# Kernel tuning notes

Hardware: AMD Instinct MI355X
Metric: run time of the kernel (lower is better)

## Reference

```python
import jax, jax.numpy as jnp
import numpy as np

N, A, M = 2, 360, 512
NP, PS = 32, 64


def _rampfilter(size):
    n = np.concatenate((np.arange(1, size / 2 + 1, 2, dtype=int),
                        np.arange(size / 2 - 1, 0, -2, dtype=int)))
    f = np.zeros(size)
    f[0] = 0.25
    f[1::2] = -1 / (np.pi * n) ** 2
    return 2 * np.real(np.fft.fft(f))


def setup_inputs() -> dict:
    rng = np.random.default_rng(0)
    sino = rng.standard_normal((N, 1, A, M))
    # ramp filtering (done in __init__ of the torch module, filtered=True)
    final_width = max(64, int(2 ** np.ceil(np.log2(2 * M))))
    pad = final_width - M
    filt = _rampfilter(final_width)
    sino_p = np.pad(sino, ((0, 0), (0, 0), (0, 0), (0, pad)))
    sino_f = np.real(np.fft.ifft(np.fft.fft(sino_p, axis=-1) * filt, axis=-1))[..., :M]
    # patch centers sampled uniformly inside the reconstruction circle
    cx, cy = [], []
    while sum(len(a) for a in cx) < NP:
        x_ = rng.random(NP) * M
        y_ = rng.random(NP) * M
        m = (x_ - M / 2) ** 2 + (y_ - M / 2) ** 2 <= (M / 2) ** 2
        cx.append(x_[m]); cy.append(y_[m])
    centers_x = np.concatenate(cx)[:NP]
    centers_y = np.concatenate(cy)[:NP]
    theta = np.linspace(0.0, np.pi, A, endpoint=False)
    return {
        'sinogram': jnp.asarray(sino_f, jnp.float32),
        'theta': jnp.asarray(theta, jnp.float32),
        'centers_x': jnp.asarray(centers_x, jnp.float32),
        'centers_y': jnp.asarray(centers_y, jnp.float32),
    }


def reference(sinogram, theta, centers_x, centers_y):
    n, _, a, m = sinogram.shape
    sino = sinogram[:, 0]                                  # (N, A, M)
    half = (m - 1) / 2.0
    x = jnp.arange(PS, dtype=sinogram.dtype) - PS / 2.0
    # patch grids (torch meshgrid 'ij'): gX varies along rows, gy along cols
    gX = (x[:, None] + jnp.zeros((PS,), sinogram.dtype)[None, :])[None] + centers_x[:, None, None]
    gy = (jnp.zeros((PS,), sinogram.dtype)[:, None] + x[None, :])[None] + centers_y[:, None, None]
    gX = gX / half - 1.0                                   # (NP, PS, PS), normalized
    gy = gy / half - 1.0
    ct, st = jnp.cos(theta), jnp.sin(theta)                # (A,)
    # rotated detector coordinate per angle: (NP, A, PS, PS)
    xg = gX[:, None] * ct[None, :, None, None] - gy[:, None] * st[None, :, None, None]
    # grid_sample bilinear along M with align_corners=True, zero padding
    u = (xg + 1.0) * half
    i0 = jnp.floor(u)
    w = u - i0
    i0i = i0.astype(jnp.int32)
    i1i = i0i + 1
    w0 = jnp.where((i0i >= 0) & (i0i <= m - 1), 1.0 - w, 0.0)
    w1 = jnp.where((i1i >= 0) & (i1i <= m - 1), w, 0.0)
    i0c = jnp.clip(i0i, 0, m - 1)
    i1c = jnp.clip(i1i, 0, m - 1)
    a_idx = jnp.arange(a)[None, :, None, None]
    g0 = sino[:, a_idx, i0c]                               # (N, NP, A, PS, PS)
    g1 = sino[:, a_idx, i1c]
    recon = (g0 * w0[None] + g1 * w1[None]).sum(axis=2)    # sum over angles -> (N, NP, PS, PS)
    mask = ((gX ** 2 + gy ** 2) <= 1.0).astype(recon.dtype)
    recon = recon * mask[None]
    return recon * (np.pi / (2.0 * a))
```

## Files before the change

### kernel.cpp

```cpp
#include <hip/hip_runtime.h>
#include <math.h>

#define N_  2
#define A_  360
#define M_  512
#define NP_ 32
#define PS_ 64
#define HALF_A 180
#define W_  24

__global__ __launch_bounds__(512) void fbp_kernel(
    const float* __restrict__ sino,
    const float* __restrict__ theta,
    const float* __restrict__ cxs,
    const float* __restrict__ cys,
    float* __restrict__ out)
{
    __shared__ float  win[A_ * W_];
    __shared__ float2 cs_tab[A_];
    __shared__ float  lo_tab[A_];
    __shared__ float  red[256];

    const float half = 255.5f;
    const int tid = threadIdx.x;

    const int bid    = blockIdx.x;
    const int region = bid & 15;
    const int p      = (bid >> 4) & (NP_ - 1);
    const int n      = bid >> 9;
    const int ri     = (region >> 2) << 4;
    const int rj     = (region &  3) << 4;

    const float cx = cxs[p];
    const float cy = cys[p];

    const float gX0 = ((float)(ri      - PS_ / 2) + cx) / half - 1.0f;
    const float gX1 = ((float)(ri + 15 - PS_ / 2) + cx) / half - 1.0f;
    const float gy0 = ((float)(rj      - PS_ / 2) + cy) / half - 1.0f;
    const float gy1 = ((float)(rj + 15 - PS_ / 2) + cy) / half - 1.0f;

    if (tid < A_) {
        const float th  = theta[tid];
        const float csx = cosf(th) * half;
        const float csy = sinf(th) * half;
        const float t0  = fmaf(-gy0, csy, half);
        const float t1  = fmaf(-gy1, csy, half);
        const float u00 = fmaf(gX0, csx, t0);
        const float u10 = fmaf(gX1, csx, t0);
        const float u01 = fmaf(gX0, csx, t1);
        const float u11 = fmaf(gX1, csx, t1);
        const float umin = fminf(fminf(u00, u10), fminf(u01, u11));
        cs_tab[tid] = make_float2(csx, csy);
        lo_tab[tid] = floorf(umin);
    }
    __syncthreads();

    const float* __restrict__ srow = sino + n * (A_ * M_);
    for (int e = tid; e < A_ * W_; e += 512) {
        const int a   = e / W_;
        const int k   = e - a * W_;
        int idx = (int)lo_tab[a] + k;
        idx = min(max(idx, 0), M_ - 1);
        win[e] = srow[a * M_ + idx];
    }
    __syncthreads();

    const int team = tid >> 8;
    const int t    = tid & 255;
    const int i    = ri + (t >> 4);
    const int j    = rj + (t & 15);

    const float gX  = ((float)(i - PS_ / 2) + cx) / half - 1.0f;
    const float gy  = ((float)(j - PS_ / 2) + cy) / half - 1.0f;
    const float ngy = -gy;

    const int a0 = team * HALF_A;
    float accG = 0.0f;
    float accW = 0.0f;
    #pragma unroll 4
    for (int a = a0; a < a0 + HALF_A; ++a) {
        const float2 cs  = cs_tab[a];
        const float  lof = lo_tab[a];
        float u = fmaf(gX, cs.x, fmaf(ngy, cs.y, half));
        u = fminf(fmaxf(u, 0.0f), 510.999f);
        const int   i0 = (int)u;
        const float w  = __builtin_amdgcn_fractf(u);
        const int   k  = i0 - (int)lof;
        const float g0 = win[a * W_ + k];
        const float g1 = win[a * W_ + k + 1];
        accG += g0;
        accW  = fmaf(w, g1 - g0, accW);
    }

    const float part = accG + accW;
    if (team == 1) red[t] = part;
    __syncthreads();
    if (team == 0) {
        const float inside = (fmaf(gX, gX, gy * gy) <= 1.0f) ? 1.0f : 0.0f;
        const float scale  = (float)(M_PI / (2.0 * (double)A_));
        out[(((n * NP_) + p) * PS_ + i) * PS_ + j] =
            (part + red[t]) * inside * scale;
    }
}

extern "C" void kernel_launch(void* const* d_in, const int* in_sizes, int n_in,
                              void* d_out, int out_size, void* d_ws, size_t ws_size,
                              hipStream_t stream) {
    const float* sino  = (const float*)d_in[0];
    const float* theta = (const float*)d_in[1];
    const float* cxs   = (const float*)d_in[2];
    const float* cys   = (const float*)d_in[3];
    float* out = (float*)d_out;

    const int blocks = N_ * NP_ * (PS_ * PS_ / 256);
    fbp_kernel<<<dim3(blocks), dim3(512), 0, stream>>>(sino, theta, cxs, cys, out);
}
```

Baseline: 35.04 us.

## Process pixel pairs per thread with float2 window and two-pass angle staging

Each thread now handles two horizontally adjacent pixels, which share a detector window lookup: the second pixel's coordinate is the first minus sin(theta), so one pair of LDS loads feeds both samples. The shared window stores (g0, g1-g0) pairs so each interpolation needs one float2 read, and angles are staged in two passes of 180 to fit the doubled window in LDS. Four thread groups split the angles, and their partial sums are reduced through LDS before a vectorized float2 store. This trades some extra staging synchronization and a select per sample for fewer LDS reads and less per-pixel address arithmetic. It relies on adjacent pixels landing in the same or the next window cell, which holds because the pixel spacing is at most one detector bin.

```diff
diff --git a/kernel.cpp b/kernel.cpp
--- a/kernel.cpp
+++ b/kernel.cpp
@@ -6,20 +6,19 @@
 #define M_  512
 #define NP_ 32
 #define PS_ 64
-#define HALF_A 180
 #define W_  24
+#define PASS_A 180
+#define CHUNK_A 45
 
-__global__ __launch_bounds__(512) void fbp_kernel(
+__global__ __launch_bounds__(512) void fbp_pair(
     const float* __restrict__ sino,
     const float* __restrict__ theta,
     const float* __restrict__ cxs,
     const float* __restrict__ cys,
     float* __restrict__ out)
 {
-    __shared__ float  win[A_ * W_];
-    __shared__ float2 cs_tab[A_];
-    __shared__ float  lo_tab[A_];
-    __shared__ float  red[256];
+    __shared__ float2 win2[PASS_A * W_];
+    __shared__ alignas(16) float4 tab[A_];
 
     const float half = 255.5f;
     const int tid = threadIdx.x;
@@ -40,66 +39,93 @@
     const float gy1 = ((float)(rj + 15 - PS_ / 2) + cy) / half - 1.0f;
 
     if (tid < A_) {
-        const float th  = theta[tid];
-        const float csx = cosf(th) * half;
-        const float csy = sinf(th) * half;
+        const float th = theta[tid];
+        const float c  = cosf(th);
+        const float s  = sinf(th);
+        const float csx = c * half;
+        const float csy = s * half;
         const float t0  = fmaf(-gy0, csy, half);
         const float t1  = fmaf(-gy1, csy, half);
         const float u00 = fmaf(gX0, csx, t0);
         const float u10 = fmaf(gX1, csx, t0);
         const float u01 = fmaf(gX0, csx, t1);
         const float u11 = fmaf(gX1, csx, t1);
-        const float umin = fminf(fminf(u00, u10), fminf(u01, u11));
-        cs_tab[tid] = make_float2(csx, csy);
-        lo_tab[tid] = floorf(umin);
+        const float lof = floorf(fminf(fminf(u00, u10), fminf(u01, u11)));
+        tab[tid] = make_float4(csx, csy, half - lof, s);
     }
     __syncthreads();
 
-    const float* __restrict__ srow = sino + n * (A_ * M_);
-    for (int e = tid; e < A_ * W_; e += 512) {
-        const int a   = e / W_;
-        const int k   = e - a * W_;
-        int idx = (int)lo_tab[a] + k;
-        idx = min(max(idx, 0), M_ - 1);
-        win[e] = srow[a * M_ + idx];
+    const int chunk = tid >> 7;
+    const int pp    = tid & 127;
+    const int i     = ri + (pp >> 3);
+    const int jp    = rj + ((pp & 7) << 1);
+
+    const float gXc  = ((float)(i  - PS_ / 2) + cx) / half - 1.0f;
+    const float gyA  = ((float)(jp - PS_ / 2) + cy) / half - 1.0f;
+    const float ngyA = -gyA;
+
+    float aG1 = 0.0f, aW1 = 0.0f;
+    float aG2 = 0.0f, aW2 = 0.0f;
+
+    for (int pass = 0; pass < 2; ++pass) {
+        const float* __restrict__ srow = sino + n * (A_ * M_) + pass * (PASS_A * M_);
+        for (int e = tid; e < PASS_A * W_; e += 512) {
+            const int al = e / W_;
+            const int k  = e - al * W_;
+            const float off = tab[pass * PASS_A + al].z;
+            const int lo = (int)(half - off);
+            const int i0 = min(max(lo + k,     0), M_ - 1);
+            const int i1 = min(max(lo + k + 1, 0), M_ - 1);
+            const float g0 = srow[al * M_ + i0];
+            const float g1 = srow[al * M_ + i1];
+            win2[e] = make_float2(g0, g1 - g0);
+        }
+        __syncthreads();
+
+        const int albase = chunk * CHUNK_A;
+        #pragma unroll 5
+        for (int q = 0; q < CHUNK_A; ++q) {
+            const float4 tb = tab[pass * PASS_A + albase + q];
+            float u1 = fmaf(gXc, tb.x, fmaf(ngyA, tb.y, tb.z));
+            float u2 = u1 - tb.w;
+            u1 = fminf(fmaxf(u1, 0.0f), 22.999f);
+            u2 = fminf(fmaxf(u2, 0.0f), 22.999f);
+            const int k1 = (int)u1;
+            const int k2 = (int)u2;
+            const float2* wrow = win2 + (albase + q) * W_;
+            const float2 P0 = wrow[k2];
+            const float2 P1 = wrow[k2 + 1];
+            const float2 Pa = (k1 != k2) ? P1 : P0;
+            const float w1 = __builtin_amdgcn_fractf(u1);
+            const float w2 = __builtin_amdgcn_fractf(u2);
+            aG1 += Pa.x;  aW1 = fmaf(w1, Pa.y, aW1);
+            aG2 += P0.x;  aW2 = fmaf(w2, P0.y, aW2);
+        }
+        __syncthreads();
+    }
+
+    float* red = (float*)win2;
+    if (chunk != 0) {
+        red[((chunk - 1) * 128 + pp) * 2 + 0] = aG1 + aW1;
+        red[((chunk - 1) * 128 + pp) * 2 + 1] = aG2 + aW2;
     }
     __syncthreads();
-
-    const int team = tid >> 8;
-    const int t    = tid & 255;
-    const int i    = ri + (t >> 4);
-    const int j    = rj + (t & 15);
-
-    const float gX  = ((float)(i - PS_ / 2) + cx) / half - 1.0f;
-    const float gy  = ((float)(j - PS_ / 2) + cy) / half - 1.0f;
-    const float ngy = -gy;
-
-    const int a0 = team * HALF_A;
-    float accG = 0.0f;
-    float accW = 0.0f;
-    #pragma unroll 4
-    for (int a = a0; a < a0 + HALF_A; ++a) {
-        const float2 cs  = cs_tab[a];
-        const float  lof = lo_tab[a];
-        float u = fmaf(gX, cs.x, fmaf(ngy, cs.y, half));
-        u = fminf(fmaxf(u, 0.0f), 510.999f);
-        const int   i0 = (int)u;
-        const float w  = __builtin_amdgcn_fractf(u);
-        const int   k  = i0 - (int)lof;
-        const float g0 = win[a * W_ + k];
-        const float g1 = win[a * W_ + k + 1];
-        accG += g0;
-        accW  = fmaf(w, g1 - g0, accW);
-    }
-
-    const float part = accG + accW;
-    if (team == 1) red[t] = part;
-    __syncthreads();
-    if (team == 0) {
-        const float inside = (fmaf(gX, gX, gy * gy) <= 1.0f) ? 1.0f : 0.0f;
-        const float scale  = (float)(M_PI / (2.0 * (double)A_));
-        out[(((n * NP_) + p) * PS_ + i) * PS_ + j] =
-            (part + red[t]) * inside * scale;
+    if (chunk == 0) {
+        float p1 = aG1 + aW1;
+        float p2 = aG2 + aW2;
+        #pragma unroll
+        for (int q = 0; q < 3; ++q) {
+            p1 += red[(q * 128 + pp) * 2 + 0];
+            p2 += red[(q * 128 + pp) * 2 + 1];
+        }
+        const float gyB = ((float)(jp + 1 - PS_ / 2) + cy) / half - 1.0f;
+        const float in1 = (fmaf(gXc, gXc, gyA * gyA) <= 1.0f) ? 1.0f : 0.0f;
+        const float in2 = (fmaf(gXc, gXc, gyB * gyB) <= 1.0f) ? 1.0f : 0.0f;
+        const float scale = (float)(M_PI / (2.0 * (double)A_));
+        float2 o;
+        o.x = p1 * in1 * scale;
+        o.y = p2 * in2 * scale;
+        *(float2*)&out[(((n * NP_) + p) * PS_ + i) * PS_ + jp] = o;
     }
 }
 
@@ -113,5 +139,5 @@
     float* out = (float*)d_out;
 
     const int blocks = N_ * NP_ * (PS_ * PS_ / 256);
-    fbp_kernel<<<dim3(blocks), dim3(512), 0, stream>>>(sino, theta, cxs, cys, out);
+    fbp_pair<<<dim3(blocks), dim3(512), 0, stream>>>(sino, theta, cxs, cys, out);
 }
```

New measurement: 31.38 us. 1.12x faster.
